# Kernel tuning notes

Measured on AMD Instinct MI355X. Metric: run time of the kernel, lower is better.

Reference implementation:

```python
import jax, jax.numpy as jnp
import numpy as np

N_VERTEX = 16384
D_IN = 128
D_OUT = 128
N_REGIONS = 64


def setup_inputs() -> dict:
    key = jax.random.key(0)
    k1, k2, k3, k4, k5 = jax.random.split(key, 5)
    h = jax.random.normal(k1, (N_VERTEX, D_IN), dtype=jnp.float32)
    # row-normalized-ish dense adjacency (small positive entries)
    norm_adj = jax.random.uniform(k2, (N_VERTEX, N_VERTEX), dtype=jnp.float32) / N_VERTEX
    region_index = jax.random.randint(k3, (N_VERTEX,), 0, N_REGIONS, dtype=jnp.int64)
    weight = jax.random.normal(k4, (D_IN, D_OUT), dtype=jnp.float32) / np.sqrt(D_IN)
    lag_weight = jax.random.normal(k5, (D_IN, D_OUT), dtype=jnp.float32) / np.sqrt(D_IN)
    reg_param = jnp.ones((N_REGIONS, D_IN), dtype=jnp.float32)
    bias = jnp.zeros((D_OUT,), dtype=jnp.float32)
    return {"h": h, "norm_adj": norm_adj, "region_index": region_index,
            "weight": weight, "lag_weight": lag_weight,
            "reg_param": reg_param, "bias": bias}


def reference(h, norm_adj, region_index, weight, lag_weight, reg_param, bias):
    # per-vertex region gather (vectorized) + elementwise mul
    reg_weight = reg_param[region_index]            # [N, d_in]
    rwh = h * reg_weight                            # [N, d_in]
    ra = rwh @ weight                               # [N, d_out]
    rb = norm_adj @ (rwh @ lag_weight)              # [N, d_out]
    return ra + rb + bias
```

## Files before the change

### kernel.cpp

```cpp
#include <hip/hip_runtime.h>
#include <hip/hip_bf16.h>

#define NV 16384
#define DD 128

typedef __attribute__((ext_vector_type(8))) short bf16x8;
typedef __attribute__((ext_vector_type(8))) unsigned short ushort8v;
typedef __attribute__((ext_vector_type(4))) float f32x4;
typedef __attribute__((ext_vector_type(2))) int i32x2;
typedef long long i64;

#define ASCALE 16384.0f
#define INV_ASCALE (1.0f / 16384.0f)

__device__ __forceinline__ unsigned short f2bf(float x) {
  unsigned u = __builtin_bit_cast(unsigned, x);
  u = (u + 0x7FFFu + ((u >> 16) & 1u)) >> 16;
  return (unsigned short)u;
}

__device__ __forceinline__ i64 pk8(f32x4 a, f32x4 b, float s) {
  int lo = 0, hi = 0;
  lo = __builtin_amdgcn_cvt_pk_fp8_f32(a[0] * s, a[1] * s, lo, false);
  lo = __builtin_amdgcn_cvt_pk_fp8_f32(a[2] * s, a[3] * s, lo, true);
  hi = __builtin_amdgcn_cvt_pk_fp8_f32(b[0] * s, b[1] * s, hi, false);
  hi = __builtin_amdgcn_cvt_pk_fp8_f32(b[2] * s, b[3] * s, hi, true);
  i32x2 r; r[0] = lo; r[1] = hi;
  return __builtin_bit_cast(i64, r);
}

__global__ __launch_bounds__(256) void k_small(
    const float* __restrict__ h, const long long* __restrict__ ridx,
    const float* __restrict__ W, const float* __restrict__ LW,
    const float* __restrict__ RP, const float* __restrict__ bias,
    float* __restrict__ ws_ra, i32x2* __restrict__ tT8)
{
  __shared__ unsigned short rw [64 * 128];
  __shared__ unsigned short Wts[128 * 128];
  __shared__ unsigned short LWts[128 * 128];
  const int tid = threadIdx.x;
  const int r0  = blockIdx.x * 64;

  {
    const int k  = tid >> 1;
    const int j0 = (tid & 1) * 64;
    const float* wr  = W  + k * DD + j0;
    const float* lwr = LW + k * DD + j0;
#pragma unroll 8
    for (int i = 0; i < 64; ++i) {
      const int j = j0 + i;
      const int off = j * 128 + (((k >> 3) ^ (j & 7)) << 3) + (k & 7);
      Wts [off] = f2bf(wr[i]);
      LWts[off] = f2bf(lwr[i]);
    }
  }

  {
    const int r  = tid >> 2;
    const int cc = tid & 3;
    const int v  = r0 + r;
    const int reg = ((int)ridx[v]) & 63;
    const float* hp = h  + (size_t)v * DD + cc * 32;
    const float* rp = RP + reg * DD + cc * 32;
#pragma unroll
    for (int i = 0; i < 4; ++i) {
      const f32x4 a  = *(const f32x4*)(hp + i * 8);
      const f32x4 b  = *(const f32x4*)(hp + i * 8 + 4);
      const f32x4 pa = *(const f32x4*)(rp + i * 8);
      const f32x4 pb = *(const f32x4*)(rp + i * 8 + 4);
      ushort8v pk;
#pragma unroll
      for (int q = 0; q < 4; ++q) {
        pk[q]     = f2bf(a[q] * pa[q]);
        pk[4 + q] = f2bf(b[q] * pb[q]);
      }
      const int sc = (cc * 4 + i) ^ (r & 7);
      *(ushort8v*)&rw[r * 128 + sc * 8] = pk;
    }
  }
  __syncthreads();

  const int w = tid >> 6, lane = tid & 63, g = lane >> 4, l15 = lane & 15;
  f32x4 accA[8], accT[8];
#pragma unroll
  for (int f = 0; f < 8; ++f) {
    accA[f] = (f32x4){0.f, 0.f, 0.f, 0.f};
    accT[f] = (f32x4){0.f, 0.f, 0.f, 0.f};
  }
  const int arow = w * 16 + l15;
#pragma unroll
  for (int s = 0; s < 4; ++s) {
    const int sca = (s * 4 + g) ^ (l15 & 7);
    const bf16x8 af = *(const bf16x8*)&rw[arow * 128 + sca * 8];
#pragma unroll
    for (int f = 0; f < 8; ++f) {
      const int j = f * 16 + l15;
      const int scb = (s * 4 + g) ^ (l15 & 7);
      const bf16x8 bw = *(const bf16x8*)&Wts [j * 128 + scb * 8];
      accA[f] = __builtin_amdgcn_mfma_f32_16x16x32_bf16(af, bw, accA[f], 0, 0, 0);
      const bf16x8 bl = *(const bf16x8*)&LWts[j * 128 + scb * 8];
      accT[f] = __builtin_amdgcn_mfma_f32_16x16x32_bf16(af, bl, accT[f], 0, 0, 0);
    }
  }

#pragma unroll
  for (int f = 0; f < 8; ++f) {
    const int col = f * 16 + l15;
    const float bj = bias[col];
#pragma unroll
    for (int q = 0; q < 4; ++q) {
      const int v = r0 + w * 16 + g * 4 + q;
      ws_ra[(size_t)v * DD + col] = accA[f][q] + bj;
    }
  }
#pragma unroll
  for (int f = 0; f < 8; ++f) {
    const int j = f * 16 + l15;
    int own = 0;
    own = __builtin_amdgcn_cvt_pk_fp8_f32(accT[f][0], accT[f][1], own, false);
    own = __builtin_amdgcn_cvt_pk_fp8_f32(accT[f][2], accT[f][3], own, true);
    const int partner = __shfl_xor(own, 16, 64);
    if ((g & 1) == 0) {
      const int v0 = r0 + w * 16 + g * 4;
      i32x2 val; val[0] = own; val[1] = partner;
      tT8[(v0 >> 6) * 1024 + ((v0 >> 3) & 7) * 128 + j] = val;
    }
  }
}

__global__ __launch_bounds__(256, 2) void k_big(
    const float* __restrict__ adj, const unsigned char* __restrict__ tTb,
    float* __restrict__ part)
{
  __shared__ unsigned char Bs[4][16384] __attribute__((aligned(16)));
  const int tid  = threadIdx.x;
  const int w    = tid >> 6;
  const int lane = tid & 63;
  const int g    = lane >> 4;
  const int l15  = lane & 15;
  const int hb   = blockIdx.x;
  const int kh   = (hb & 7) >> 2;
  const int mblk = (hb >> 3) * 4 + (hb & 3);
  const int bid  = mblk * 2 + kh;
  const int r0   = mblk * 64;
  const int t0   = mblk & 63;
  const int arow = r0 + w * 16 + l15;
  const float* abase = adj + (size_t)arow * NV + kh * (NV / 2) + g * 8;
  const unsigned char* bbase = tTb + (size_t)kh * 128 * 8192;

#define RT(t) ((t0 + (t)) & 63)

  f32x4 acc[8];
#pragma unroll
  for (int f = 0; f < 8; ++f) acc[f] = (f32x4){0.f, 0.f, 0.f, 0.f};

  f32x4 A0[8], A1[8];

#define STAGE(slot, rt) do {                                                   \
    const int buf_ = (slot) & 3;                                               \
    _Pragma("unroll")                                                          \
    for (int i_ = 0; i_ < 4; ++i_) {                                           \
      const int unit_ = i_ * 4 + w;                                            \
      const unsigned char* src_ = bbase + (size_t)(rt) * 16384 +               \
                                  unit_ * 1024 + lane * 16;                    \
      __builtin_amdgcn_global_load_lds(                                        \
          (const __attribute__((address_space(1))) unsigned int*)src_,         \
          (__attribute__((address_space(3))) unsigned int*)&Bs[buf_][unit_ * 1024], \
          16, 0, 0);                                                           \
    } } while (0)

#define LOADA(AS, rt) do {                                                     \
    _Pragma("unroll")                                                          \
    for (int s_ = 0; s_ < 4; ++s_) {                                           \
      const f32x4* p_ = (const f32x4*)(abase + (size_t)(rt) * 128 + s_ * 32);  \
      AS[2 * s_]     = p_[0];                                                  \
      AS[2 * s_ + 1] = p_[1];                                                  \
    } } while (0)

#define COMP(AS, slot) do {                                                    \
    const int buf_ = (slot) & 3;                                               \
    const i64 a0_ = pk8(AS[0], AS[1], ASCALE);                                 \
    const i64 a1_ = pk8(AS[2], AS[3], ASCALE);                                 \
    const i64 a2_ = pk8(AS[4], AS[5], ASCALE);                                 \
    const i64 a3_ = pk8(AS[6], AS[7], ASCALE);                                 \
    _Pragma("unroll")                                                          \
    for (int f_ = 0; f_ < 8; ++f_) {                                           \
      const int jr8_ = (f_ * 16 + l15) * 8;                                    \
      acc[f_] = __builtin_amdgcn_mfma_f32_16x16x32_fp8_fp8(a0_,                \
          *(const i64*)&Bs[buf_][g * 1024 + jr8_],            acc[f_], 0, 0, 0); \
      acc[f_] = __builtin_amdgcn_mfma_f32_16x16x32_fp8_fp8(a1_,                \
          *(const i64*)&Bs[buf_][(4 + g) * 1024 + jr8_],      acc[f_], 0, 0, 0); \
      acc[f_] = __builtin_amdgcn_mfma_f32_16x16x32_fp8_fp8(a2_,                \
          *(const i64*)&Bs[buf_][8192 + g * 1024 + jr8_],     acc[f_], 0, 0, 0); \
      acc[f_] = __builtin_amdgcn_mfma_f32_16x16x32_fp8_fp8(a3_,                \
          *(const i64*)&Bs[buf_][8192 + (4 + g) * 1024 + jr8_], acc[f_], 0, 0, 0); \
    } } while (0)

#define VW12 asm volatile("s_waitcnt vmcnt(12)" ::: "memory")
#define VW0  asm volatile("s_waitcnt vmcnt(0)"  ::: "memory")
#define BAR  __builtin_amdgcn_s_barrier()

  STAGE(0, RT(0)); LOADA(A0, RT(0));
  STAGE(1, RT(1)); LOADA(A1, RT(1));

  for (int tp = 0; tp < 31; ++tp) {
    const int t = tp * 2;
    VW12; BAR; STAGE(t + 2, RT(t + 2)); COMP(A0, t);     LOADA(A0, RT(t + 2));
    VW12; BAR; STAGE(t + 3, RT(t + 3)); COMP(A1, t + 1); LOADA(A1, RT(t + 3));
  }
  VW12; BAR; COMP(A0, 62);
  VW0;  BAR; COMP(A1, 63);

#undef STAGE
#undef LOADA
#undef COMP
#undef VW12
#undef VW0
#undef BAR
#undef RT

  float* pbase = part + ((size_t)bid * 64 + w * 16) * DD;
#pragma unroll
  for (int f = 0; f < 8; ++f) {
    const int col = f * 16 + l15;
#pragma unroll
    for (int q = 0; q < 4; ++q) {
      const int row = g * 4 + q;
      pbase[row * DD + col] = acc[f][q];
    }
  }
}

__global__ __launch_bounds__(256) void k_reduce(
    const float* __restrict__ part, const float* __restrict__ ws_ra,
    float* __restrict__ out)
{
  const size_t e = ((size_t)blockIdx.x * 256 + threadIdx.x) * 4;
  const int    mblk  = (int)(e >> 13);
  const int    local = (int)(e & 8191);
  const f32x4 p0 = *(const f32x4*)&part[(size_t)(2 * mblk)     * 8192 + local];
  const f32x4 p1 = *(const f32x4*)&part[(size_t)(2 * mblk + 1) * 8192 + local];
  const f32x4 ra = *(const f32x4*)&ws_ra[e];
  f32x4 o;
#pragma unroll
  for (int i = 0; i < 4; ++i) o[i] = (p0[i] + p1[i]) * INV_ASCALE + ra[i];
  *(f32x4*)&out[e] = o;
}

extern "C" void kernel_launch(void* const* d_in, const int* in_sizes, int n_in,
                              void* d_out, int out_size, void* d_ws, size_t ws_size,
                              hipStream_t stream) {
  const float*     h    = (const float*)d_in[0];
  const float*     adj  = (const float*)d_in[1];
  const long long* ridx = (const long long*)d_in[2];
  const float*     W    = (const float*)d_in[3];
  const float*     LW   = (const float*)d_in[4];
  const float*     RP   = (const float*)d_in[5];
  const float*     bias = (const float*)d_in[6];
  float* out = (float*)d_out;

  float* ws_ra = (float*)d_ws;
  void*  tT8   = (void*)((char*)d_ws + (size_t)8  * 1024 * 1024);
  float* part  = (float*)((char*)d_ws + (size_t)16 * 1024 * 1024);

  hipLaunchKernelGGL(k_small, dim3(NV / 64), dim3(256), 0, stream,
                     h, ridx, W, LW, RP, bias, ws_ra, (i32x2*)tT8);
  hipLaunchKernelGGL(k_big, dim3(NV / 64 * 2), dim3(256), 0, stream,
                     adj, (const unsigned char*)tT8, part);
  hipLaunchKernelGGL(k_reduce, dim3((NV * DD / 4) / 256), dim3(256), 0, stream,
                     part, ws_ra, out);
}
```

Baseline: 228.9 us.

## Split K four ways in big GEMM with triple-buffered A loads

The dense adjacency GEMM now splits the K dimension into four parts instead of two. That doubles the grid to 1024 blocks and halves the per-block shared tile to 32 KB, so launch bounds rise to 4 blocks per CU. Each step loads and computes half as much K, and the register A-prefetch moves from double to triple buffering. The reduce kernel now sums four partials, which adds partial-buffer traffic in exchange for more occupancy and deeper latency hiding on the streaming adjacency reads.

```diff
diff --git a/kernel.cpp b/kernel.cpp
--- a/kernel.cpp
+++ b/kernel.cpp
@@ -128,25 +128,25 @@
   }
 }
 
-__global__ __launch_bounds__(256, 2) void k_big(
+__global__ __launch_bounds__(256, 4) void k_big(
     const float* __restrict__ adj, const unsigned char* __restrict__ tTb,
     float* __restrict__ part)
 {
-  __shared__ unsigned char Bs[4][16384] __attribute__((aligned(16)));
+  __shared__ unsigned char Bs[4][8192] __attribute__((aligned(16)));
   const int tid  = threadIdx.x;
   const int w    = tid >> 6;
   const int lane = tid & 63;
   const int g    = lane >> 4;
   const int l15  = lane & 15;
   const int hb   = blockIdx.x;
-  const int kh   = (hb & 7) >> 2;
-  const int mblk = (hb >> 3) * 4 + (hb & 3);
-  const int bid  = mblk * 2 + kh;
+  const int kh   = (hb & 7) >> 1;
+  const int mblk = (hb >> 3) * 2 + (hb & 1);
+  const int bid  = mblk * 4 + kh;
   const int r0   = mblk * 64;
   const int t0   = mblk & 63;
   const int arow = r0 + w * 16 + l15;
-  const float* abase = adj + (size_t)arow * NV + kh * (NV / 2) + g * 8;
-  const unsigned char* bbase = tTb + (size_t)kh * 128 * 8192;
+  const float* abase = adj + (size_t)arow * NV + kh * (NV / 4) + g * 8;
+  const unsigned char* bbase = tTb + (size_t)kh * 64 * 8192;
 
 #define RT(t) ((t0 + (t)) & 63)
 
@@ -154,14 +154,14 @@
 #pragma unroll
   for (int f = 0; f < 8; ++f) acc[f] = (f32x4){0.f, 0.f, 0.f, 0.f};
 
-  f32x4 A0[8], A1[8];
+  f32x4 A0[4], A1[4], A2[4];
 
 #define STAGE(slot, rt) do {                                                   \
     const int buf_ = (slot) & 3;                                               \
     _Pragma("unroll")                                                          \
-    for (int i_ = 0; i_ < 4; ++i_) {                                           \
-      const int unit_ = i_ * 4 + w;                                            \
-      const unsigned char* src_ = bbase + (size_t)(rt) * 16384 +               \
+    for (int i_ = 0; i_ < 2; ++i_) {                                           \
+      const int unit_ = i_ * 4 + w;                    \
+      const unsigned char* src_ = bbase + (size_t)(rt) * 8192 +                \
                                   unit_ * 1024 + lane * 16;                    \
       __builtin_amdgcn_global_load_lds(                                        \
           (const __attribute__((address_space(1))) unsigned int*)src_,         \
@@ -170,51 +170,52 @@
     } } while (0)
 
 #define LOADA(AS, rt) do {                                                     \
-    _Pragma("unroll")                                                          \
-    for (int s_ = 0; s_ < 4; ++s_) {                                           \
-      const f32x4* p_ = (const f32x4*)(abase + (size_t)(rt) * 128 + s_ * 32);  \
-      AS[2 * s_]     = p_[0];                                                  \
-      AS[2 * s_ + 1] = p_[1];                                                  \
-    } } while (0)
+    const f32x4* p_ = (const f32x4*)(abase + (size_t)(rt) * 64);               \
+    AS[0] = p_[0];                                                             \
+    AS[1] = p_[1];                                                             \
+    const f32x4* q_ = (const f32x4*)(abase + (size_t)(rt) * 64 + 32);          \
+    AS[2] = q_[0];                                                             \
+    AS[3] = q_[1];                                                             \
+  } while (0)
 
 #define COMP(AS, slot) do {                                                    \
     const int buf_ = (slot) & 3;                                               \
     const i64 a0_ = pk8(AS[0], AS[1], ASCALE);                                 \
     const i64 a1_ = pk8(AS[2], AS[3], ASCALE);                                 \
-    const i64 a2_ = pk8(AS[4], AS[5], ASCALE);                                 \
-    const i64 a3_ = pk8(AS[6], AS[7], ASCALE);                                 \
     _Pragma("unroll")                                                          \
     for (int f_ = 0; f_ < 8; ++f_) {                                           \
       const int jr8_ = (f_ * 16 + l15) * 8;                                    \
       acc[f_] = __builtin_amdgcn_mfma_f32_16x16x32_fp8_fp8(a0_,                \
-          *(const i64*)&Bs[buf_][g * 1024 + jr8_],            acc[f_], 0, 0, 0); \
+          *(const i64*)&Bs[buf_][g * 1024 + jr8_],       acc[f_], 0, 0, 0);    \
       acc[f_] = __builtin_amdgcn_mfma_f32_16x16x32_fp8_fp8(a1_,                \
-          *(const i64*)&Bs[buf_][(4 + g) * 1024 + jr8_],      acc[f_], 0, 0, 0); \
-      acc[f_] = __builtin_amdgcn_mfma_f32_16x16x32_fp8_fp8(a2_,                \
-          *(const i64*)&Bs[buf_][8192 + g * 1024 + jr8_],     acc[f_], 0, 0, 0); \
-      acc[f_] = __builtin_amdgcn_mfma_f32_16x16x32_fp8_fp8(a3_,                \
-          *(const i64*)&Bs[buf_][8192 + (4 + g) * 1024 + jr8_], acc[f_], 0, 0, 0); \
+          *(const i64*)&Bs[buf_][(4 + g) * 1024 + jr8_], acc[f_], 0, 0, 0);    \
     } } while (0)
 
 #define VW12 asm volatile("s_waitcnt vmcnt(12)" ::: "memory")
+#define VW6  asm volatile("s_waitcnt vmcnt(6)"  ::: "memory")
 #define VW0  asm volatile("s_waitcnt vmcnt(0)"  ::: "memory")
 #define BAR  __builtin_amdgcn_s_barrier()
 
   STAGE(0, RT(0)); LOADA(A0, RT(0));
   STAGE(1, RT(1)); LOADA(A1, RT(1));
-
-  for (int tp = 0; tp < 31; ++tp) {
-    const int t = tp * 2;
-    VW12; BAR; STAGE(t + 2, RT(t + 2)); COMP(A0, t);     LOADA(A0, RT(t + 2));
-    VW12; BAR; STAGE(t + 3, RT(t + 3)); COMP(A1, t + 1); LOADA(A1, RT(t + 3));
-  }
-  VW12; BAR; COMP(A0, 62);
-  VW0;  BAR; COMP(A1, 63);
+  STAGE(2, RT(2)); LOADA(A2, RT(2));
+
+  for (int tq = 0; tq < 20; ++tq) {
+    const int t = tq * 3;
+    VW12; BAR; STAGE(t + 3, RT(t + 3)); COMP(A0, t);     LOADA(A0, RT(t + 3));
+    VW12; BAR; STAGE(t + 4, RT(t + 4)); COMP(A1, t + 1); LOADA(A1, RT(t + 4));
+    VW12; BAR; STAGE(t + 5, RT(t + 5)); COMP(A2, t + 2); LOADA(A2, RT(t + 5));
+  }
+  VW12; BAR; STAGE(63, RT(63)); COMP(A0, 60); LOADA(A0, RT(63));
+  VW12; BAR; COMP(A1, 61);
+  VW6;  BAR; COMP(A2, 62);
+  VW0;  BAR; COMP(A0, 63);
 
 #undef STAGE
 #undef LOADA
 #undef COMP
 #undef VW12
+#undef VW6
 #undef VW0
 #undef BAR
 #undef RT
@@ -238,12 +239,15 @@
   const size_t e = ((size_t)blockIdx.x * 256 + threadIdx.x) * 4;
   const int    mblk  = (int)(e >> 13);
   const int    local = (int)(e & 8191);
-  const f32x4 p0 = *(const f32x4*)&part[(size_t)(2 * mblk)     * 8192 + local];
-  const f32x4 p1 = *(const f32x4*)&part[(size_t)(2 * mblk + 1) * 8192 + local];
+  const f32x4 p0 = *(const f32x4*)&part[(size_t)(4 * mblk)     * 8192 + local];
+  const f32x4 p1 = *(const f32x4*)&part[(size_t)(4 * mblk + 1) * 8192 + local];
+  const f32x4 p2 = *(const f32x4*)&part[(size_t)(4 * mblk + 2) * 8192 + local];
+  const f32x4 p3 = *(const f32x4*)&part[(size_t)(4 * mblk + 3) * 8192 + local];
   const f32x4 ra = *(const f32x4*)&ws_ra[e];
   f32x4 o;
 #pragma unroll
-  for (int i = 0; i < 4; ++i) o[i] = (p0[i] + p1[i]) * INV_ASCALE + ra[i];
+  for (int i = 0; i < 4; ++i)
+    o[i] = (((p0[i] + p1[i]) + p2[i]) + p3[i]) * INV_ASCALE + ra[i];
   *(f32x4*)&out[e] = o;
 }
 
@@ -265,7 +269,7 @@
 
   hipLaunchKernelGGL(k_small, dim3(NV / 64), dim3(256), 0, stream,
                      h, ridx, W, LW, RP, bias, ws_ra, (i32x2*)tT8);
-  hipLaunchKernelGGL(k_big, dim3(NV / 64 * 2), dim3(256), 0, stream,
+  hipLaunchKernelGGL(k_big, dim3(NV / 64 * 4), dim3(256), 0, stream,
                      adj, (const unsigned char*)tT8, part);
   hipLaunchKernelGGL(k_reduce, dim3((NV * DD / 4) / 256), dim3(256), 0, stream,
                      part, ws_ra, out);
```

After: 245.5 us. +7.3%, slower.

## Stage adjacency tiles through LDS with swizzle and triple-buffered 64-wide K steps

Applied to the files above, without the earlier changes.

The fp32 adjacency tiles now go to LDS through direct global-to-LDS async loads, using an XOR column swizzle, instead of register prefetch. They are read back from LDS before fp8 packing. The K step shrinks from 128 to 64 columns, and the ring becomes three 24 KB buffers (A plus B) instead of four B-only buffers, with the wait counts adjusted to match. The aim is to free registers and keep more loads in flight asynchronously, at the cost of extra LDS traffic and twice as many barriers per K.

```diff
diff --git a/kernel.cpp b/kernel.cpp
--- a/kernel.cpp
+++ b/kernel.cpp
@@ -132,7 +132,7 @@
     const float* __restrict__ adj, const unsigned char* __restrict__ tTb,
     float* __restrict__ part)
 {
-  __shared__ unsigned char Bs[4][16384] __attribute__((aligned(16)));
+  __shared__ unsigned char Bs[3][24576] __attribute__((aligned(16)));
   const int tid  = threadIdx.x;
   const int w    = tid >> 6;
   const int lane = tid & 63;
@@ -143,78 +143,81 @@
   const int mblk = (hb >> 3) * 4 + (hb & 3);
   const int bid  = mblk * 2 + kh;
   const int r0   = mblk * 64;
-  const int t0   = mblk & 63;
-  const int arow = r0 + w * 16 + l15;
-  const float* abase = adj + (size_t)arow * NV + kh * (NV / 2) + g * 8;
+  const int t0   = mblk & 127;
   const unsigned char* bbase = tTb + (size_t)kh * 128 * 8192;
 
-#define RT(t) ((t0 + (t)) & 63)
+#define RT(t) ((t0 + (t)) & 127)
+
+  const float* asrc[4];
+#pragma unroll
+  for (int i = 0; i < 4; ++i) {
+    const int rrel = w * 16 + i * 4 + (lane >> 4);
+    const int cswz = (lane & 15) ^ ((i * 4 + (lane >> 4)) & 7);
+    asrc[i] = adj + (size_t)(r0 + rrel) * NV + kh * (NV / 2) + cswz * 4;
+  }
 
   f32x4 acc[8];
 #pragma unroll
   for (int f = 0; f < 8; ++f) acc[f] = (f32x4){0.f, 0.f, 0.f, 0.f};
 
-  f32x4 A0[8], A1[8];
-
-#define STAGE(slot, rt) do {                                                   \
-    const int buf_ = (slot) & 3;                                               \
+#define STAGE(bufidx, rt) do {                                                 \
     _Pragma("unroll")                                                          \
-    for (int i_ = 0; i_ < 4; ++i_) {                                           \
+    for (int i_ = 0; i_ < 4; ++i_) {      \
+      const float* srcA_ = asrc[i_] + (size_t)(rt) * 64;                       \
+      unsigned char* dstA_ = &Bs[bufidx][(w * 16 + i_ * 4) * 256];             \
+      __builtin_amdgcn_global_load_lds(                                        \
+          (const __attribute__((address_space(1))) unsigned int*)srcA_,        \
+          (__attribute__((address_space(3))) unsigned int*)dstA_, 16, 0, 0);   \
+    }                                                                          \
+    _Pragma("unroll")                                                          \
+    for (int i_ = 0; i_ < 2; ++i_) {                          \
       const int unit_ = i_ * 4 + w;                                            \
-      const unsigned char* src_ = bbase + (size_t)(rt) * 16384 +               \
-                                  unit_ * 1024 + lane * 16;                    \
+      const unsigned char* srcB_ = bbase + (size_t)(rt) * 8192 +               \
+                                   unit_ * 1024 + lane * 16;                   \
+      unsigned char* dstB_ = &Bs[bufidx][16384 + unit_ * 1024];                \
       __builtin_amdgcn_global_load_lds(                                        \
-          (const __attribute__((address_space(1))) unsigned int*)src_,         \
-          (__attribute__((address_space(3))) unsigned int*)&Bs[buf_][unit_ * 1024], \
-          16, 0, 0);                                                           \
+          (const __attribute__((address_space(1))) unsigned int*)srcB_,        \
+          (__attribute__((address_space(3))) unsigned int*)dstB_, 16, 0, 0);   \
     } } while (0)
 
-#define LOADA(AS, rt) do {                                                     \
-    _Pragma("unroll")                                                          \
-    for (int s_ = 0; s_ < 4; ++s_) {                                           \
-      const f32x4* p_ = (const f32x4*)(abase + (size_t)(rt) * 128 + s_ * 32);  \
-      AS[2 * s_]     = p_[0];                                                  \
-      AS[2 * s_ + 1] = p_[1];                                                  \
-    } } while (0)
-
-#define COMP(AS, slot) do {                                                    \
-    const int buf_ = (slot) & 3;                                               \
-    const i64 a0_ = pk8(AS[0], AS[1], ASCALE);                                 \
-    const i64 a1_ = pk8(AS[2], AS[3], ASCALE);                                 \
-    const i64 a2_ = pk8(AS[4], AS[5], ASCALE);                                 \
-    const i64 a3_ = pk8(AS[6], AS[7], ASCALE);                                 \
+#define COMP(bufidx) do {                                                      \
+    const unsigned char* Ab_ = &Bs[bufidx][(w * 16 + l15) * 256];              \
+    const int x_ = l15 & 7;                                                    \
+    const f32x4 c0_ = *(const f32x4*)&Ab_[((2 * g)     ^ x_) * 16];            \
+    const f32x4 c1_ = *(const f32x4*)&Ab_[((2 * g + 1) ^ x_) * 16];            \
+    const f32x4 c2_ = *(const f32x4*)&Ab_[((8 + 2 * g)     ^ x_) * 16];        \
+    const f32x4 c3_ = *(const f32x4*)&Ab_[((8 + 2 * g + 1) ^ x_) * 16];        \
+    const i64 a0_ = pk8(c0_, c1_, ASCALE);                                     \
+    const i64 a1_ = pk8(c2_, c3_, ASCALE);                                     \
+    const unsigned char* Bb_ = &Bs[bufidx][16384];                             \
     _Pragma("unroll")                                                          \
     for (int f_ = 0; f_ < 8; ++f_) {                                           \
       const int jr8_ = (f_ * 16 + l15) * 8;                                    \
       acc[f_] = __builtin_amdgcn_mfma_f32_16x16x32_fp8_fp8(a0_,                \
-          *(const i64*)&Bs[buf_][g * 1024 + jr8_],            acc[f_], 0, 0, 0); \
+          *(const i64*)&Bb_[g * 1024 + jr8_],       acc[f_], 0, 0, 0);         \
       acc[f_] = __builtin_amdgcn_mfma_f32_16x16x32_fp8_fp8(a1_,                \
-          *(const i64*)&Bs[buf_][(4 + g) * 1024 + jr8_],      acc[f_], 0, 0, 0); \
-      acc[f_] = __builtin_amdgcn_mfma_f32_16x16x32_fp8_fp8(a2_,                \
-          *(const i64*)&Bs[buf_][8192 + g * 1024 + jr8_],     acc[f_], 0, 0, 0); \
-      acc[f_] = __builtin_amdgcn_mfma_f32_16x16x32_fp8_fp8(a3_,                \
-          *(const i64*)&Bs[buf_][8192 + (4 + g) * 1024 + jr8_], acc[f_], 0, 0, 0); \
+          *(const i64*)&Bb_[(4 + g) * 1024 + jr8_], acc[f_], 0, 0, 0);         \
     } } while (0)
 
-#define VW12 asm volatile("s_waitcnt vmcnt(12)" ::: "memory")
-#define VW0  asm volatile("s_waitcnt vmcnt(0)"  ::: "memory")
+#define VW6  asm volatile("s_waitcnt vmcnt(6)" ::: "memory")
+#define VW0  asm volatile("s_waitcnt vmcnt(0)" ::: "memory")
 #define BAR  __builtin_amdgcn_s_barrier()
 
-  STAGE(0, RT(0)); LOADA(A0, RT(0));
-  STAGE(1, RT(1)); LOADA(A1, RT(1));
-
-  for (int tp = 0; tp < 31; ++tp) {
-    const int t = tp * 2;
-    VW12; BAR; STAGE(t + 2, RT(t + 2)); COMP(A0, t);     LOADA(A0, RT(t + 2));
-    VW12; BAR; STAGE(t + 3, RT(t + 3)); COMP(A1, t + 1); LOADA(A1, RT(t + 3));
-  }
-  VW12; BAR; COMP(A0, 62);
-  VW0;  BAR; COMP(A1, 63);
+  STAGE(0, RT(0));
+  STAGE(1, RT(1));
+
+  for (int tq = 0; tq < 42; ++tq) {
+    const int t = tq * 3;
+    VW6; BAR; STAGE(2, RT(t + 2)); COMP(0);
+    VW6; BAR; STAGE(0, RT(t + 3)); COMP(1);
+    VW6; BAR; STAGE(1, RT(t + 4)); COMP(2);
+  }
+  VW6; BAR; COMP(0);
+  VW0; BAR; COMP(1);
 
 #undef STAGE
-#undef LOADA
 #undef COMP
-#undef VW12
+#undef VW6
 #undef VW0
 #undef BAR
 #undef RT
```

New measurement: 218.9 us. 4.4% less time.
